# Optimization experiments

Hardware: AMD Instinct MI355X
Metric: run time of the kernel (lower is better)

Reference implementation:

```python
import jax, jax.numpy as jnp
import numpy as np

DIM = 128
HEADS = 32
DIM_HEAD = 64
INNER = DIM * DIM_HEAD  # 8192, as written in the source (dim * dim_head)
D = INNER // HEADS      # 256 per-head dim
B, N = 1, 2048
ROT = 64                # partial rotary width (l)
SCALE = DIM ** (-0.5)   # source uses dim**-0.5, not head-dim


def _rotate_half(x):
    # x: [..., l]; split as (j d) with j=2 -> cat(-x2, x1)
    x1, x2 = jnp.split(x, 2, axis=-1)
    return jnp.concatenate((-x2, x1), axis=-1)


def _apply_rotary(q, k, freqs):
    # freqs: [n, l]; q,k: [b,h,n,d] with l <= d (partial rotary)
    l = freqs.shape[-1]
    cos, sin = jnp.cos(freqs), jnp.sin(freqs)  # broadcast over b,h
    ql, qr = q[..., :l], q[..., l:]
    kl, kr = k[..., :l], k[..., l:]
    ql = ql * cos + _rotate_half(ql) * sin
    kl = kl * cos + _rotate_half(kl) * sin
    return jnp.concatenate((ql, qr), axis=-1), jnp.concatenate((kl, kr), axis=-1)


def setup_inputs() -> dict:
    key = jax.random.key(0)
    k1, k2, k3, k4, k5 = jax.random.split(key, 5)
    return {
        "x": jax.random.normal(k1, (B, N, DIM), dtype=jnp.float32),
        "Wqkv": jax.random.normal(k2, (3 * INNER, DIM), dtype=jnp.float32) * 0.02,
        "Wproj": jax.random.normal(k3, (DIM, INNER), dtype=jnp.float32) * 0.02,
        "bproj": jax.random.normal(k4, (DIM,), dtype=jnp.float32) * 0.02,
        "rotary_pos_emb": jax.random.normal(k5, (N, ROT), dtype=jnp.float32),
    }


def reference(x, Wqkv, Wproj, bproj, rotary_pos_emb):
    b, n, _ = x.shape
    qkv = x @ Wqkv.T                                   # [b, n, 3*inner]
    qkv = qkv.reshape(b, n, 3, HEADS, D)               # (qkv h d) ordering
    qkv = jnp.transpose(qkv, (2, 0, 3, 1, 4))          # [3, b, h, n, d]
    q, k, v = qkv[0], qkv[1], qkv[2]
    q, k = _apply_rotary(q, k, rotary_pos_emb)
    energy = jnp.einsum("bhid,bhjd->bhij", q, k) * SCALE  # [b,h,n,n]
    attn = jax.nn.softmax(energy, axis=-1)
    out = jnp.einsum("bhij,bhjd->bhid", attn, v)       # [b,h,n,d]
    out = jnp.transpose(out, (0, 2, 1, 3)).reshape(b, n, INNER)
    return out @ Wproj.T + bproj
```

## Files before the change

kernel.cpp:

```cpp
#include <hip/hip_runtime.h>


typedef unsigned short u16;
typedef unsigned int u32;
typedef __attribute__((ext_vector_type(8))) u16 u16x8;
typedef __attribute__((ext_vector_type(8))) __bf16 bf16x8;
typedef __attribute__((ext_vector_type(4))) float f32x4;
typedef __attribute__((ext_vector_type(2))) u32 u32x2;

#define DEV static __device__ __forceinline__

DEV u16 f2b(float f) {
  u32 u = __builtin_bit_cast(u32, f);
  u += 0x7fffu + ((u >> 16) & 1u);
  return (u16)(u >> 16);
}
DEV float b2f(u16 b) {
  u32 u = ((u32)b) << 16;
  return __builtin_bit_cast(float, u);
}
DEV u32 pack2(float a, float b) { return (u32)f2b(a) | ((u32)f2b(b) << 16); }

DEV f32x4 mfma16(u16x8 a, u16x8 b, f32x4 c) {
  return __builtin_amdgcn_mfma_f32_16x16x32_bf16(
      __builtin_bit_cast(bf16x8, a), __builtin_bit_cast(bf16x8, b), c, 0, 0, 0);
}

DEV int swz(int row, int kelem, int rowBytes) {
  return row * rowBytes + ((kelem * 2) ^ ((row & 7) << 4));
}

DEV void dma16(const void* g, void* l) {
  __builtin_amdgcn_global_load_lds(
      (const __attribute__((address_space(1))) void*)g,
      (__attribute__((address_space(3))) void*)l, 16, 0, 0);
}

__global__ __launch_bounds__(256) void k_cvt(const float* __restrict__ src,
                                             u16* __restrict__ dst, int n8) {
  int i = blockIdx.x * 256 + threadIdx.x;
  if (i >= n8) return;
  const float4* s = (const float4*)src;
  float4 a = s[i * 2], b = s[i * 2 + 1];
  u16x8 o;
  o[0] = f2b(a.x); o[1] = f2b(a.y); o[2] = f2b(a.z); o[3] = f2b(a.w);
  o[4] = f2b(b.x); o[5] = f2b(b.y); o[6] = f2b(b.z); o[7] = f2b(b.w);
  *(u16x8*)(dst + (size_t)i * 8) = o;
}

__global__ __launch_bounds__(256) void k_qkv(const u16* __restrict__ xb,
                                             const u16* __restrict__ wb,
                                             u16* __restrict__ qw,
                                             u16* __restrict__ kw,
                                             u16* __restrict__ vw) {
  __shared__ char lds[65536];
  const int tid = threadIdx.x;
  const int rt = blockIdx.x % 192, nt = blockIdx.x / 192;
  const int r0 = rt * 128, n0 = nt * 128;
#pragma unroll
  for (int p = 0; p < 8; ++p) {
    int row = p * 16 + (tid >> 4);
    int k0 = (tid & 15) * 8;
    *(u16x8*)(lds + swz(row, k0, 256)) =
        *(const u16x8*)(wb + (size_t)(r0 + row) * 128 + k0);
    *(u16x8*)(lds + 32768 + swz(row, k0, 256)) =
        *(const u16x8*)(xb + (size_t)(n0 + row) * 128 + k0);
  }
  __syncthreads();
  const int wid = tid >> 6, lane = tid & 63, lq = lane & 15, g = lane >> 4;
  const int wr = wid >> 1, wn = wid & 1;
  const bool isV = (r0 >= 16384);
  f32x4 acc[4][4] = {};
#pragma unroll
  for (int ks = 0; ks < 4; ++ks) {
    u16x8 wa[4], xa[4];
#pragma unroll
    for (int i = 0; i < 4; ++i) {
      int rw = wr * 64 + i * 16 + lq;
      wa[i] = *(const u16x8*)(lds + swz(rw, ks * 32 + g * 8, 256));
      int rx = wn * 64 + i * 16 + lq;
      xa[i] = *(const u16x8*)(lds + 32768 + swz(rx, ks * 32 + g * 8, 256));
    }
    if (!isV) {
#pragma unroll
      for (int i = 0; i < 4; ++i)
#pragma unroll
        for (int j = 0; j < 4; ++j) acc[i][j] = mfma16(wa[i], xa[j], acc[i][j]);
    } else {
#pragma unroll
      for (int i = 0; i < 4; ++i)
#pragma unroll
        for (int j = 0; j < 4; ++j) acc[i][j] = mfma16(xa[j], wa[i], acc[i][j]);
    }
  }
  if (!isV) {
#pragma unroll
    for (int i = 0; i < 4; ++i) {
      int rb = r0 + wr * 64 + i * 16 + g * 4;
      u16* dst0 = (rb >= 8192) ? kw : qw;
      int hd = rb & 8191;
      int h = hd >> 8, db = hd & 255;
#pragma unroll
      for (int j = 0; j < 4; ++j) {
        int n = n0 + wn * 64 + j * 16 + lq;
        u32x2 pk;
        pk.x = pack2(acc[i][j][0], acc[i][j][1]);
        pk.y = pack2(acc[i][j][2], acc[i][j][3]);
        *(u32x2*)(dst0 + ((size_t)h * 2048 + n) * 256 + db) = pk;
      }
    }
  } else {
#pragma unroll
    for (int i = 0; i < 4; ++i) {
      int rc = r0 - 16384 + wr * 64 + i * 16 + lq;
      int h = rc >> 8, d = rc & 255;
#pragma unroll
      for (int j = 0; j < 4; ++j) {
        int nb = n0 + wn * 64 + j * 16 + g * 4;
        u32x2 pk;
        pk.x = pack2(acc[i][j][0], acc[i][j][1]);
        pk.y = pack2(acc[i][j][2], acc[i][j][3]);
        *(u32x2*)(vw + ((size_t)h * 256 + d) * 2048 + nb) = pk;
      }
    }
  }
}

__global__ __launch_bounds__(256) void k_rope(u16* __restrict__ qw,
                                              u16* __restrict__ kw,
                                              const float* __restrict__ fr) {
  int idx = blockIdx.x * 256 + threadIdx.x;
  int seg = idx & 3;
  int n = (idx >> 2) & 2047;
  int h = (idx >> 13) & 31;
  u16* base = ((idx >> 18) ? kw : qw) + ((size_t)h * 2048 + n) * 256 + seg * 8;
  u16x8 lo = *(const u16x8*)base;
  u16x8 hi = *(const u16x8*)(base + 32);
  const float* f = fr + n * 64 + seg * 8;
  u16x8 nlo, nhi;
#pragma unroll
  for (int e = 0; e < 8; ++e) {
    float fl = f[e], fh = f[e + 32];
    float sl, cl, sh, ch;
    sincosf(fl, &sl, &cl);
    sincosf(fh, &sh, &ch);
    float a = b2f(lo[e]), b = b2f(hi[e]);
    nlo[e] = f2b(a * cl - b * sl);
    nhi[e] = f2b(b * ch + a * sh);
  }
  *(u16x8*)base = nlo;
  *(u16x8*)(base + 32) = nhi;
}

__global__ __launch_bounds__(512, 2) void k_attn(const u16* __restrict__ qw,
                                                 const u16* __restrict__ kw,
                                                 const u16* __restrict__ vw,
                                                 u16* __restrict__ ow) {
  __shared__ char lds[65536];
  const int tid = threadIdx.x;
  const int j = blockIdx.x & 31;
  const int h = (j & 7) * 4 + (j >> 3);
  const int qb = blockIdx.x >> 5;
  const int wid = tid >> 6, lane = tid & 63, lq = lane & 15, g = lane >> 4;
  const int q0 = qb * 256 + wid * 32;
  const float SM = 0.08838834764831845f * 1.4426950408889634f;

  const u16* kbase = kw + (size_t)h * 2048 * 256;
  const u16* vbase = vw + (size_t)h * 256 * 2048;

  int kro[2], kgo[2];
#pragma unroll
  for (int i = 0; i < 2; ++i) {
    int r = wid * 4 + 2 * i + (lane >> 5);
    kro[i] = r;
    kgo[i] = r * 256 + (((lane & 31) ^ (r & 7)) * 8);
  }
  int vgo[2];
#pragma unroll
  for (int i = 0; i < 2; ++i) {
    int L = wid * 16 + 8 * i + (lane >> 3);
    int l = (lane & 7) ^ (L & 7);
    int d = 2 * L + (l >> 2);
    vgo[i] = d * 2048 + (l & 3) * 8;
  }

  u16x8 qf[2][8];
  {
    const u16* q0p = qw + ((size_t)h * 2048 + q0 + lq) * 256;
#pragma unroll
    for (int ds = 0; ds < 8; ++ds) {
      qf[0][ds] = *(const u16x8*)(q0p + ds * 32 + g * 8);
      qf[1][ds] = *(const u16x8*)(q0p + 16 * 256 + ds * 32 + g * 8);
    }
  }

  f32x4 oacc[2][16] = {};
  float mrun[2] = {-1e30f, -1e30f}, lrun[2] = {0.f, 0.f};

#define STAGE(T)                                                         \
  {                                                                      \
    const int kv0 = (T) * 32;                                            \
    char* kb = lds + ((T) & 1) * 32768;                                  \
    char* vb = kb + 16384;                                               \
    dma16(kbase + (size_t)kv0 * 256 + kgo[0], kb + (wid * 4) * 512);     \
    dma16(kbase + (size_t)kv0 * 256 + kgo[1], kb + (wid * 4 + 2) * 512); \
    dma16(vbase + (size_t)kv0 + vgo[0], vb + (wid * 16) * 128);          \
    dma16(vbase + (size_t)kv0 + vgo[1], vb + (wid * 16 + 8) * 128);     \
  }

  STAGE(0);

  for (int t = 0; t < 64; ++t) {
    if (t < 63) {
      STAGE(t + 1);
      asm volatile("s_waitcnt vmcnt(4)" ::: "memory");
    } else {
      asm volatile("s_waitcnt vmcnt(0)" ::: "memory");
    }
    __builtin_amdgcn_s_barrier();
    asm volatile("" ::: "memory");

    const char* kb = lds + (t & 1) * 32768;
    const char* vb = kb + 16384;

    f32x4 sa[2][2] = {};
    __builtin_amdgcn_s_setprio(1);
#pragma unroll
    for (int ds = 0; ds < 8; ++ds) {
#pragma unroll
      for (int f = 0; f < 2; ++f) {
        int kr = f * 16 + lq;
        u16x8 ka = *(const u16x8*)(kb + kr * 512 +
                                   ((((ds << 2) | g) ^ (kr & 7)) << 4));
        sa[0][f] = mfma16(ka, qf[0][ds], sa[0][f]);
        sa[1][f] = mfma16(ka, qf[1][ds], sa[1][f]);
      }
    }
    __builtin_amdgcn_s_setprio(0);

    u32 pk[2][2][2];
#pragma unroll
    for (int c = 0; c < 2; ++c) {
      float ps[2][4];
      float mt = -1e30f;
#pragma unroll
      for (int f = 0; f < 2; ++f)
#pragma unroll
        for (int r = 0; r < 4; ++r) {
          ps[f][r] = sa[c][f][r] * SM;
          mt = fmaxf(mt, ps[f][r]);
        }
      mt = fmaxf(mt, __shfl_xor(mt, 16));
      mt = fmaxf(mt, __shfl_xor(mt, 32));
      bool skip = __all(mt - mrun[c] <= 8.0f);
      if (!skip) {
        float mnew = fmaxf(mrun[c], mt);
        float corr = exp2f(mrun[c] - mnew);
        lrun[c] *= corr;
#pragma unroll
        for (int di = 0; di < 16; ++di) {
          oacc[c][di][0] *= corr; oacc[c][di][1] *= corr;
          oacc[c][di][2] *= corr; oacc[c][di][3] *= corr;
        }
        mrun[c] = mnew;
      }
      float lt = 0.f;
#pragma unroll
      for (int f = 0; f < 2; ++f) {
        float p0 = exp2f(ps[f][0] - mrun[c]);
        float p1 = exp2f(ps[f][1] - mrun[c]);
        float p2 = exp2f(ps[f][2] - mrun[c]);
        float p3 = exp2f(ps[f][3] - mrun[c]);
        lt += (p0 + p1) + (p2 + p3);
        pk[c][f][0] = pack2(p0, p1);
        pk[c][f][1] = pack2(p2, p3);
      }
      lt += __shfl_xor(lt, 16);
      lt += __shfl_xor(lt, 32);
      lrun[c] += lt;
    }

    u16x8 pb[2];
#pragma unroll
    for (int c = 0; c < 2; ++c) {
      u32 bu[4];
#pragma unroll
      for (int tt = 0; tt < 4; ++tt) {
        int src = (2 * (g & 1) + (tt >> 1)) * 16 + lq;
        u32 vlo = (u32)__shfl((int)pk[c][0][tt & 1], src);
        u32 vhi = (u32)__shfl((int)pk[c][1][tt & 1], src);
        bu[tt] = (g < 2) ? vlo : vhi;
      }
#pragma unroll
      for (int tt = 0; tt < 4; ++tt) {
        pb[c][2 * tt] = (u16)(bu[tt] & 0xffff);
        pb[c][2 * tt + 1] = (u16)(bu[tt] >> 16);
      }
    }

    __builtin_amdgcn_s_setprio(1);
#pragma unroll
    for (int di = 0; di < 16; ++di) {
      int dr = di * 16 + lq;
      int L = dr >> 1;
      u16x8 va = *(const u16x8*)(
          vb + L * 128 + ((((((dr & 1) << 2) | g) ^ (L & 7))) << 4));
      oacc[0][di] = mfma16(va, pb[0], oacc[0][di]);
      oacc[1][di] = mfma16(va, pb[1], oacc[1][di]);
    }
    __builtin_amdgcn_s_setprio(0);

    __builtin_amdgcn_s_barrier();
    asm volatile("" ::: "memory");
  }
#undef STAGE

#pragma unroll
  for (int c = 0; c < 2; ++c) {
    float inv = 1.0f / lrun[c];
    u16* orow = ow + (size_t)(q0 + c * 16 + lq) * 8192 + h * 256;
#pragma unroll
    for (int di = 0; di < 16; ++di) {
      u32x2 o2;
      o2.x = pack2(oacc[c][di][0] * inv, oacc[c][di][1] * inv);
      o2.y = pack2(oacc[c][di][2] * inv, oacc[c][di][3] * inv);
      *(u32x2*)(orow + di * 16 + g * 4) = o2;
    }
  }
}

__global__ __launch_bounds__(256) void k_proj(const u16* __restrict__ ow,
                                              const u16* __restrict__ wp,
                                              float* __restrict__ part) {
  __shared__ char lds[49152];
  const int tid = threadIdx.x;
  const int nt = blockIdx.x >> 3, kc = blockIdx.x & 7;
  const int n0 = nt * 64, kb = kc * 1024;
  const int wid = tid >> 6, lane = tid & 63, lq = lane & 15, g = lane >> 4;
  f32x4 acc[8] = {};
  for (int kt = 0; kt < 8; ++kt) {
    int kk = kb + kt * 128;
#pragma unroll
    for (int p = 0; p < 4; ++p) {
      int nr = p * 16 + (tid >> 4);
      int k0 = (tid & 15) * 8;
      *(u16x8*)(lds + swz(nr, k0, 256)) =
          *(const u16x8*)(ow + (size_t)(n0 + nr) * 8192 + kk + k0);
    }
#pragma unroll
    for (int p = 0; p < 8; ++p) {
      int er = p * 16 + (tid >> 4);
      int k0 = (tid & 15) * 8;
      *(u16x8*)(lds + 16384 + swz(er, k0, 256)) =
          *(const u16x8*)(wp + (size_t)er * 8192 + kk + k0);
    }
    __syncthreads();
#pragma unroll
    for (int ks = 0; ks < 4; ++ks) {
      int nr = wid * 16 + lq;
      u16x8 oa = *(const u16x8*)(lds + swz(nr, ks * 32 + g * 8, 256));
#pragma unroll
      for (int ef = 0; ef < 8; ++ef) {
        int er = ef * 16 + lq;
        u16x8 wf = *(const u16x8*)(lds + 16384 + swz(er, ks * 32 + g * 8, 256));
        acc[ef] = mfma16(oa, wf, acc[ef]);
      }
    }
    __syncthreads();
  }
  float* pb = part + (size_t)kc * 262144;
#pragma unroll
  for (int ef = 0; ef < 8; ++ef)
#pragma unroll
    for (int r = 0; r < 4; ++r) {
      int n = n0 + wid * 16 + g * 4 + r;
      pb[n * 128 + ef * 16 + lq] = acc[ef][r];
    }
}

__global__ __launch_bounds__(256) void k_reduce(const float* __restrict__ part,
                                                const float* __restrict__ bias,
                                                float* __restrict__ out) {
  int i = blockIdx.x * 256 + threadIdx.x;
  float s = bias[i & 127];
#pragma unroll
  for (int c = 0; c < 8; ++c) s += part[(size_t)c * 262144 + i];
  out[i] = s;
}

extern "C" void kernel_launch(void* const* d_in, const int* in_sizes, int n_in,
                              void* d_out, int out_size, void* d_ws, size_t ws_size,
                              hipStream_t stream) {
  const float* x = (const float*)d_in[0];
  const float* wqkv = (const float*)d_in[1];
  const float* wproj = (const float*)d_in[2];
  const float* bproj = (const float*)d_in[3];
  const float* rope = (const float*)d_in[4];
  char* ws = (char*)d_ws;
  u16* xb    = (u16*)(ws);
  u16* wqkvb = (u16*)(ws + 524288);
  u16* wpb   = (u16*)(ws + 6815744);
  u16* qw    = (u16*)(ws + 8912896);
  u16* kw    = (u16*)(ws + 42467328);
  u16* vw    = (u16*)(ws + 76021760);
  u16* owv   = (u16*)(ws + 109576192);
  float* part = (float*)(ws + 8912896);

  k_cvt<<<128, 256, 0, stream>>>(x, xb, 32768);
  k_cvt<<<1536, 256, 0, stream>>>(wqkv, wqkvb, 393216);
  k_cvt<<<512, 256, 0, stream>>>(wproj, wpb, 131072);
  k_qkv<<<3072, 256, 0, stream>>>(xb, wqkvb, qw, kw, vw);
  k_rope<<<2048, 256, 0, stream>>>(qw, kw, rope);
  k_attn<<<256, 512, 0, stream>>>(qw, kw, vw, owv);
  k_proj<<<256, 256, 0, stream>>>(owv, wpb, part);
  k_reduce<<<1024, 256, 0, stream>>>(part, bproj, (float*)d_out);
}
```

Measured before the change: 269.8 us.

## Shrink attention blocks, fold softmax scale into Q, use fast bf16 and sincos

The attention kernel now runs 256-thread blocks covering 128 queries each, with twice as many blocks. Each wave issues four K/V DMA loads per stage, and the LDS swizzle shrinks to a 4-way XOR so read offsets can be precomputed once. The softmax scale times log2(e) is folded into Q at the QKV-projection epilogue, removing a per-score multiply. Separately, bf16 conversion uses the native cast, rope uses fast __sincosf, and P packing becomes a bit-cast. The costs are reduced sincos precision, a different bf16 rounding path, more K/V reloads across blocks, and possibly more LDS bank conflicts from the narrower swizzle.

```diff
diff --git a/kernel.cpp b/kernel.cpp
--- a/kernel.cpp
+++ b/kernel.cpp
@@ -6,20 +6,20 @@
 typedef __attribute__((ext_vector_type(8))) u16 u16x8;
 typedef __attribute__((ext_vector_type(8))) __bf16 bf16x8;
 typedef __attribute__((ext_vector_type(4))) float f32x4;
+typedef __attribute__((ext_vector_type(4))) u32 u32x4;
 typedef __attribute__((ext_vector_type(2))) u32 u32x2;
 
 #define DEV static __device__ __forceinline__
 
 DEV u16 f2b(float f) {
-  u32 u = __builtin_bit_cast(u32, f);
-  u += 0x7fffu + ((u >> 16) & 1u);
-  return (u16)(u >> 16);
+  __bf16 h = (__bf16)f;
+  return __builtin_bit_cast(u16, h);
 }
 DEV float b2f(u16 b) {
   u32 u = ((u32)b) << 16;
   return __builtin_bit_cast(float, u);
 }
-DEV u32 pack2(float a, float b) { return (u32)f2b(a) | ((u32)f2b(b) << 16); }
+DEV u32 pk2(float a, float b) { return (u32)f2b(a) | ((u32)f2b(b) << 16); }
 
 DEV f32x4 mfma16(u16x8 a, u16x8 b, f32x4 c) {
   return __builtin_amdgcn_mfma_f32_16x16x32_bf16(
@@ -93,19 +93,21 @@
         for (int j = 0; j < 4; ++j) acc[i][j] = mfma16(xa[j], wa[i], acc[i][j]);
     }
   }
+  const float SMQ = 0.08838834764831845f * 1.4426950408889634f;
   if (!isV) {
 #pragma unroll
     for (int i = 0; i < 4; ++i) {
       int rb = r0 + wr * 64 + i * 16 + g * 4;
       u16* dst0 = (rb >= 8192) ? kw : qw;
+      float scl = (rb >= 8192) ? 1.0f : SMQ;
       int hd = rb & 8191;
       int h = hd >> 8, db = hd & 255;
 #pragma unroll
       for (int j = 0; j < 4; ++j) {
         int n = n0 + wn * 64 + j * 16 + lq;
         u32x2 pk;
-        pk.x = pack2(acc[i][j][0], acc[i][j][1]);
-        pk.y = pack2(acc[i][j][2], acc[i][j][3]);
+        pk.x = pk2(acc[i][j][0] * scl, acc[i][j][1] * scl);
+        pk.y = pk2(acc[i][j][2] * scl, acc[i][j][3] * scl);
         *(u32x2*)(dst0 + ((size_t)h * 2048 + n) * 256 + db) = pk;
       }
     }
@@ -118,8 +120,8 @@
       for (int j = 0; j < 4; ++j) {
         int nb = n0 + wn * 64 + j * 16 + g * 4;
         u32x2 pk;
-        pk.x = pack2(acc[i][j][0], acc[i][j][1]);
-        pk.y = pack2(acc[i][j][2], acc[i][j][3]);
+        pk.x = pk2(acc[i][j][0], acc[i][j][1]);
+        pk.y = pk2(acc[i][j][2], acc[i][j][3]);
         *(u32x2*)(vw + ((size_t)h * 256 + d) * 2048 + nb) = pk;
       }
     }
@@ -142,8 +144,8 @@
   for (int e = 0; e < 8; ++e) {
     float fl = f[e], fh = f[e + 32];
     float sl, cl, sh, ch;
-    sincosf(fl, &sl, &cl);
-    sincosf(fh, &sh, &ch);
+    __sincosf(fl, &sl, &cl);
+    __sincosf(fh, &sh, &ch);
     float a = b2f(lo[e]), b = b2f(hi[e]);
     nlo[e] = f2b(a * cl - b * sl);
     nhi[e] = f2b(b * ch + a * sh);
@@ -152,37 +154,35 @@
   *(u16x8*)(base + 32) = nhi;
 }
 
-__global__ __launch_bounds__(512, 2) void k_attn(const u16* __restrict__ qw,
+__global__ __launch_bounds__(256, 2) void k_attn(const u16* __restrict__ qw,
                                                  const u16* __restrict__ kw,
                                                  const u16* __restrict__ vw,
                                                  u16* __restrict__ ow) {
   __shared__ char lds[65536];
   const int tid = threadIdx.x;
   const int j = blockIdx.x & 31;
-  const int h = (j & 7) * 4 + (j >> 3);
+  const int h = j;
   const int qb = blockIdx.x >> 5;
   const int wid = tid >> 6, lane = tid & 63, lq = lane & 15, g = lane >> 4;
-  const int q0 = qb * 256 + wid * 32;
-  const float SM = 0.08838834764831845f * 1.4426950408889634f;
+  const int q0 = qb * 128 + wid * 32;
 
   const u16* kbase = kw + (size_t)h * 2048 * 256;
   const u16* vbase = vw + (size_t)h * 256 * 2048;
 
-  int kro[2], kgo[2];
-#pragma unroll
-  for (int i = 0; i < 2; ++i) {
-    int r = wid * 4 + 2 * i + (lane >> 5);
-    kro[i] = r;
-    kgo[i] = r * 256 + (((lane & 31) ^ (r & 7)) * 8);
-  }
-  int vgo[2];
-#pragma unroll
-  for (int i = 0; i < 2; ++i) {
-    int L = wid * 16 + 8 * i + (lane >> 3);
-    int l = (lane & 7) ^ (L & 7);
-    int d = 2 * L + (l >> 2);
-    vgo[i] = d * 2048 + (l & 3) * 8;
-  }
+  int kgo[4], vgo[4];
+#pragma unroll
+  for (int i = 0; i < 4; ++i) {
+    int r = wid * 8 + 2 * i + (lane >> 5);
+    kgo[i] = r * 256 + (((lane & 31) ^ (r & 3)) * 8);
+    int L = wid * 32 + 8 * i + (lane >> 3);
+    int cs = (lane & 7) ^ (L & 3);
+    int d = 2 * L + (cs >> 2);
+    vgo[i] = d * 2048 + (cs & 3) * 8;
+  }
+
+  const int kread = lq * 512 + ((g ^ (lq & 3)) << 4);
+  const int vread = 16384 + (lq >> 1) * 128 + ((lq & 1) << 6)
+                    + ((g ^ ((lq >> 1) & 3)) << 4);
 
   u16x8 qf[2][8];
   {
@@ -197,15 +197,16 @@
   f32x4 oacc[2][16] = {};
   float mrun[2] = {-1e30f, -1e30f}, lrun[2] = {0.f, 0.f};
 
-#define STAGE(T)                                                         \
-  {                                                                      \
-    const int kv0 = (T) * 32;                                            \
-    char* kb = lds + ((T) & 1) * 32768;                                  \
-    char* vb = kb + 16384;                                               \
-    dma16(kbase + (size_t)kv0 * 256 + kgo[0], kb + (wid * 4) * 512);     \
-    dma16(kbase + (size_t)kv0 * 256 + kgo[1], kb + (wid * 4 + 2) * 512); \
-    dma16(vbase + (size_t)kv0 + vgo[0], vb + (wid * 16) * 128);          \
-    dma16(vbase + (size_t)kv0 + vgo[1], vb + (wid * 16 + 8) * 128);     \
+#define STAGE(T)                                                          \
+  {                                                                       \
+    const int kv0 = (T) * 32;                                             \
+    char* kb_ = lds + ((T) & 1) * 32768;                                  \
+    char* vb_ = kb_ + 16384;                                              \
+    _Pragma("unroll") for (int i = 0; i < 4; ++i) {                       \
+      dma16(kbase + (size_t)kv0 * 256 + kgo[i],                           \
+            kb_ + (wid * 8 + 2 * i) * 512);                               \
+      dma16(vbase + (size_t)kv0 + vgo[i], vb_ + (wid * 32 + 8 * i) * 128);\
+    }                                                                     \
   }
 
   STAGE(0);
@@ -213,7 +214,7 @@
   for (int t = 0; t < 64; ++t) {
     if (t < 63) {
       STAGE(t + 1);
-      asm volatile("s_waitcnt vmcnt(4)" ::: "memory");
+      asm volatile("s_waitcnt vmcnt(8)" ::: "memory");
     } else {
       asm volatile("s_waitcnt vmcnt(0)" ::: "memory");
     }
@@ -221,7 +222,6 @@
     asm volatile("" ::: "memory");
 
     const char* kb = lds + (t & 1) * 32768;
-    const char* vb = kb + 16384;
 
     f32x4 sa[2][2] = {};
     __builtin_amdgcn_s_setprio(1);
@@ -229,9 +229,7 @@
     for (int ds = 0; ds < 8; ++ds) {
 #pragma unroll
       for (int f = 0; f < 2; ++f) {
-        int kr = f * 16 + lq;
-        u16x8 ka = *(const u16x8*)(kb + kr * 512 +
-                                   ((((ds << 2) | g) ^ (kr & 7)) << 4));
+        u16x8 ka = *(const u16x8*)(kb + kread + f * 8192 + ds * 64);
         sa[0][f] = mfma16(ka, qf[0][ds], sa[0][f]);
         sa[1][f] = mfma16(ka, qf[1][ds], sa[1][f]);
       }
@@ -241,15 +239,11 @@
     u32 pk[2][2][2];
 #pragma unroll
     for (int c = 0; c < 2; ++c) {
-      float ps[2][4];
       float mt = -1e30f;
 #pragma unroll
       for (int f = 0; f < 2; ++f)
 #pragma unroll
-        for (int r = 0; r < 4; ++r) {
-          ps[f][r] = sa[c][f][r] * SM;
-          mt = fmaxf(mt, ps[f][r]);
-        }
+        for (int r = 0; r < 4; ++r) mt = fmaxf(mt, sa[c][f][r]);
       mt = fmaxf(mt, __shfl_xor(mt, 16));
       mt = fmaxf(mt, __shfl_xor(mt, 32));
       bool skip = __all(mt - mrun[c] <= 8.0f);
@@ -267,13 +261,13 @@
       float lt = 0.f;
 #pragma unroll
       for (int f = 0; f < 2; ++f) {
-        float p0 = exp2f(ps[f][0] - mrun[c]);
-        float p1 = exp2f(ps[f][1] - mrun[c]);
-        float p2 = exp2f(ps[f][2] - mrun[c]);
-        float p3 = exp2f(ps[f][3] - mrun[c]);
+        float p0 = exp2f(sa[c][f][0] - mrun[c]);
+        float p1 = exp2f(sa[c][f][1] - mrun[c]);
+        float p2 = exp2f(sa[c][f][2] - mrun[c]);
+        float p3 = exp2f(sa[c][f][3] - mrun[c]);
         lt += (p0 + p1) + (p2 + p3);
-        pk[c][f][0] = pack2(p0, p1);
-        pk[c][f][1] = pack2(p2, p3);
+        pk[c][f][0] = pk2(p0, p1);
+        pk[c][f][1] = pk2(p2, p3);
       }
       lt += __shfl_xor(lt, 16);
       lt += __shfl_xor(lt, 32);
@@ -283,7 +277,7 @@
     u16x8 pb[2];
 #pragma unroll
     for (int c = 0; c < 2; ++c) {
-      u32 bu[4];
+      u32x4 bu;
 #pragma unroll
       for (int tt = 0; tt < 4; ++tt) {
         int src = (2 * (g & 1) + (tt >> 1)) * 16 + lq;
@@ -291,20 +285,13 @@
         u32 vhi = (u32)__shfl((int)pk[c][1][tt & 1], src);
         bu[tt] = (g < 2) ? vlo : vhi;
       }
-#pragma unroll
-      for (int tt = 0; tt < 4; ++tt) {
-        pb[c][2 * tt] = (u16)(bu[tt] & 0xffff);
-        pb[c][2 * tt + 1] = (u16)(bu[tt] >> 16);
-      }
+      pb[c] = __builtin_bit_cast(u16x8, bu);
     }
 
     __builtin_amdgcn_s_setprio(1);
 #pragma unroll
     for (int di = 0; di < 16; ++di) {
-      int dr = di * 16 + lq;
-      int L = dr >> 1;
-      u16x8 va = *(const u16x8*)(
-          vb + L * 128 + ((((((dr & 1) << 2) | g) ^ (L & 7))) << 4));
+      u16x8 va = *(const u16x8*)(kb + vread + di * 1024);
       oacc[0][di] = mfma16(va, pb[0], oacc[0][di]);
       oacc[1][di] = mfma16(va, pb[1], oacc[1][di]);
     }
@@ -322,8 +309,8 @@
 #pragma unroll
     for (int di = 0; di < 16; ++di) {
       u32x2 o2;
-      o2.x = pack2(oacc[c][di][0] * inv, oacc[c][di][1] * inv);
-      o2.y = pack2(oacc[c][di][2] * inv, oacc[c][di][3] * inv);
+      o2.x = pk2(oacc[c][di][0] * inv, oacc[c][di][1] * inv);
+      o2.y = pk2(oacc[c][di][2] * inv, oacc[c][di][3] * inv);
       *(u32x2*)(orow + di * 16 + g * 4) = o2;
     }
   }
@@ -411,7 +398,7 @@
   k_cvt<<<512, 256, 0, stream>>>(wproj, wpb, 131072);
   k_qkv<<<3072, 256, 0, stream>>>(xb, wqkvb, qw, kw, vw);
   k_rope<<<2048, 256, 0, stream>>>(qw, kw, rope);
-  k_attn<<<256, 512, 0, stream>>>(qw, kw, vw, owv);
+  k_attn<<<512, 256, 0, stream>>>(qw, kw, vw, owv);
   k_proj<<<256, 256, 0, stream>>>(owv, wpb, part);
   k_reduce<<<1024, 256, 0, stream>>>(part, bproj, (float*)d_out);
 }
```

Measured after the change: 265.8 us. Within noise of the previous version (-1.5%).
